# Kernel optimization log

Hardware: AMD Instinct MI355X
Metric: run time of the kernel (lower is better)

## Reference

```python
import jax, jax.numpy as jnp
import numpy as np

D_MODEL = 2048
NUM_HEADS = 16
D_KV = D_MODEL // NUM_HEADS
THETA = 10000.0


def apply_rope(x, pos):
    # x: [B, H, S, d_kv], pos: [S] int
    d = x.shape[-1]
    inv_freq = 1.0 / (THETA ** (jnp.arange(0, d, 2, dtype=jnp.float32) / d))  # [d/2]
    ang = pos.astype(jnp.float32)[:, None] * inv_freq[None, :]  # [S, d/2]
    cos, sin = jnp.cos(ang), jnp.sin(ang)  # broadcast over B,H
    x1 = x[..., 0::2]
    x2 = x[..., 1::2]
    r1 = x1 * cos - x2 * sin
    r2 = x1 * sin + x2 * cos
    return jnp.stack([r1, r2], axis=-1).reshape(x.shape)


def setup_inputs() -> dict:
    key = jax.random.key(0)
    k = jax.random.split(key, 5)
    B, S = 2, 2048
    x = jax.random.normal(k[0], (B, S, D_MODEL), dtype=jnp.float32)
    scale = 1.0 / np.sqrt(D_MODEL)
    Wq = jax.random.normal(k[1], (D_MODEL, D_MODEL), dtype=jnp.float32) * scale
    Wk = jax.random.normal(k[2], (D_MODEL, D_MODEL), dtype=jnp.float32) * scale
    Wv = jax.random.normal(k[3], (D_MODEL, D_MODEL), dtype=jnp.float32) * scale
    Wo = jax.random.normal(k[4], (D_MODEL, D_MODEL), dtype=jnp.float32) * scale
    token_position = jnp.arange(S, dtype=jnp.int64 if jax.config.jax_enable_x64 else jnp.int32)
    return {"x": x, "Wq": Wq, "Wk": Wk, "Wv": Wv, "Wo": Wo, "token_position": token_position}


def reference(x, Wq, Wk, Wv, Wo, token_position):
    B, S, _ = x.shape
    def heads(y):
        return y.reshape(B, S, NUM_HEADS, D_KV).transpose(0, 2, 1, 3)  # [B,H,S,d]
    Q = heads(jnp.einsum('bsd,df->bsf', x, Wq))
    K = heads(jnp.einsum('bsd,df->bsf', x, Wk))
    V = heads(jnp.einsum('bsd,df->bsf', x, Wv))
    Q = apply_rope(Q, token_position)
    K = apply_rope(K, token_position)
    scale = 1.0 / jnp.sqrt(jnp.asarray(D_KV, dtype=x.dtype))
    scores = jnp.einsum('bhqd,bhkd->bhqk', Q, K) * scale  # [B,H,S,S]
    causal = jnp.tril(jnp.ones((S, S), dtype=bool))
    scores = jnp.where(causal, scores, -jnp.inf)
    attn = jax.nn.softmax(scores, axis=-1)
    out = jnp.einsum('bhqk,bhkd->bhqd', attn, V)  # [B,H,S,d]
    out = out.transpose(0, 2, 1, 3).reshape(B, S, D_MODEL)
    return jnp.einsum('bsd,df->bsf', out, Wo)
```

## Files before the change

### kernel.cpp

```cpp
#include <hip/hip_runtime.h>
#include <hip/hip_bf16.h>

#define S 2048
#define DM 2048
#define NH 16
#define DH 128

typedef __attribute__((ext_vector_type(8))) short short8;
typedef __attribute__((ext_vector_type(4))) float floatx4;
typedef unsigned short u16;
typedef unsigned int u32;

__device__ __forceinline__ u16 f2bf(float f) {
  union { float f; u32 u; } v; v.f = f;
  u32 r = v.u + 0x7fffu + ((v.u >> 16) & 1u);
  return (u16)(r >> 16);
}
__device__ __forceinline__ u32 pack2(float lo, float hi) {
  float2 f; f.x = lo; f.y = hi;
  __hip_bfloat162 h = __float22bfloat162_rn(f);
  union { __hip_bfloat162 h; u32 u; } c; c.h = h;
  return c.u;
}

__device__ __forceinline__ floatx4 mfma16(short8 a, short8 b, floatx4 c) {
  return __builtin_amdgcn_mfma_f32_16x16x32_bf16(a, b, c, 0, 0, 0);
}

__device__ __forceinline__ void async_cp16(const u16* g, u16* l) {
  __builtin_amdgcn_global_load_lds(
      (const __attribute__((address_space(1))) void*)g,
      (__attribute__((address_space(3))) void*)l, 16, 0, 0);
}

__global__ void conv_x_k(const float* __restrict__ x, u16* __restrict__ xb) {
  int gid = blockIdx.x * 256 + threadIdx.x;
  float4 v = ((const float4*)x)[gid];
  uint2 p; p.x = pack2(v.x, v.y); p.y = pack2(v.z, v.w);
  ((uint2*)xb)[gid] = p;
}

__global__ void conv_w_k(const float* __restrict__ W0, const float* __restrict__ W1,
                         const float* __restrict__ W2, const float* __restrict__ W3,
                         u16* __restrict__ out) {
  __shared__ float tile[32][33];
  const float* W = blockIdx.z == 0 ? W0 : blockIdx.z == 1 ? W1 : blockIdx.z == 2 ? W2 : W3;
  u16* O = out + (size_t)blockIdx.z * DM * DM;
  int tx = threadIdx.x & 31, ty = threadIdx.x >> 5;
  int k0 = blockIdx.y * 32, n0 = blockIdx.x * 32;
#pragma unroll
  for (int j = 0; j < 4; j++)
    tile[ty + j * 8][tx] = W[(size_t)(k0 + ty + j * 8) * DM + n0 + tx];
  __syncthreads();
#pragma unroll
  for (int j = 0; j < 4; j++)
    O[(size_t)(n0 + ty + j * 8) * DM + k0 + tx] = f2bf(tile[tx][ty + j * 8]);
}

#define BM 128
#define BN 256
#define BK 64
#define NT (DM / BK)

#define BARRIER __builtin_amdgcn_s_barrier()
#define SB __builtin_amdgcn_sched_barrier(0)
#define LGKM0 asm volatile("s_waitcnt lgkmcnt(0)" ::: "memory")

#define STG_B(q, j, koff) \
  async_cp16(pBg + (size_t)(j) * 32 * DM + (koff), &Bs[q][so + (j) * 2048])
#define STG_A(q, j, koff) \
  async_cp16(pAg + (size_t)(j) * 32 * DM + (koff), &As[q][so + (j) * 2048])

#define MFMA4(mi, av) \
    acc[mi][0] = mfma16(av, b0, acc[mi][0]); \
    acc[mi][1] = mfma16(av, b1, acc[mi][1]); \
    acc[mi][2] = mfma16(av, b2, acc[mi][2]); \
    acc[mi][3] = mfma16(av, b3, acc[mi][3]);

#define PH1(p, q, koff, PRE) { \
    a0 = *(const short8*)&As[p][arow + xk0]; \
    a1 = *(const short8*)&As[p][1024 + arow + xk0]; \
    a2 = *(const short8*)&As[p][2048 + arow + xk0]; \
    a3 = *(const short8*)&As[p][3072 + arow + xk0]; \
    b0 = *(const short8*)&Bs[p][brow + xk0]; \
    b1 = *(const short8*)&Bs[p][1024 + brow + xk0]; \
    b2 = *(const short8*)&Bs[p][2048 + brow + xk0]; \
    b3 = *(const short8*)&Bs[p][3072 + brow + xk0]; \
    if (PRE) { STG_B(q, 0, koff); STG_B(q, 1, koff); STG_B(q, 2, koff); } \
    BARRIER; LGKM0; SB; \
    __builtin_amdgcn_s_setprio(1); \
    MFMA4(0, a0) MFMA4(1, a1) MFMA4(2, a2) MFMA4(3, a3) \
    __builtin_amdgcn_s_setprio(0); SB; \
    if (PRE) { asm volatile("s_waitcnt vmcnt(3)" ::: "memory"); } \
    else     { asm volatile("s_waitcnt vmcnt(0)" ::: "memory"); } \
    BARRIER; }

#define PH2(p, q, koff, PRE) { \
    a0 = *(const short8*)&As[p][4096 + arow + xk0]; \
    a1 = *(const short8*)&As[p][5120 + arow + xk0]; \
    a2 = *(const short8*)&As[p][6144 + arow + xk0]; \
    a3 = *(const short8*)&As[p][7168 + arow + xk0]; \
    if (PRE) { STG_B(q, 3, koff); STG_B(q, 4, koff); STG_B(q, 5, koff); } \
    BARRIER; LGKM0; SB; \
    __builtin_amdgcn_s_setprio(1); \
    MFMA4(4, a0) MFMA4(5, a1) MFMA4(6, a2) MFMA4(7, a3) \
    __builtin_amdgcn_s_setprio(0); \
    BARRIER; }

#define PH3(p, q, koff, PRE) { \
    a0 = *(const short8*)&As[p][arow + xk1]; \
    a1 = *(const short8*)&As[p][1024 + arow + xk1]; \
    a2 = *(const short8*)&As[p][2048 + arow + xk1]; \
    a3 = *(const short8*)&As[p][3072 + arow + xk1]; \
    b0 = *(const short8*)&Bs[p][brow + xk1]; \
    b1 = *(const short8*)&Bs[p][1024 + brow + xk1]; \
    b2 = *(const short8*)&Bs[p][2048 + brow + xk1]; \
    b3 = *(const short8*)&Bs[p][3072 + brow + xk1]; \
    if (PRE) { STG_B(q, 6, koff); STG_B(q, 7, koff); STG_A(q, 0, koff); } \
    BARRIER; LGKM0; SB; \
    __builtin_amdgcn_s_setprio(1); \
    MFMA4(0, a0) MFMA4(1, a1) MFMA4(2, a2) MFMA4(3, a3) \
    __builtin_amdgcn_s_setprio(0); \
    BARRIER; }

#define PH4(p, q, koff, PRE, LAST) { \
    a0 = *(const short8*)&As[p][4096 + arow + xk1]; \
    a1 = *(const short8*)&As[p][5120 + arow + xk1]; \
    a2 = *(const short8*)&As[p][6144 + arow + xk1]; \
    a3 = *(const short8*)&As[p][7168 + arow + xk1]; \
    if (PRE) { STG_A(q, 1, koff); STG_A(q, 2, koff); STG_A(q, 3, koff); } \
    BARRIER; LGKM0; SB; \
    __builtin_amdgcn_s_setprio(1); \
    MFMA4(4, a0) MFMA4(5, a1) MFMA4(6, a2) MFMA4(7, a3) \
    __builtin_amdgcn_s_setprio(0); SB; \
    if (!LAST) { asm volatile("s_waitcnt vmcnt(2)" ::: "memory"); BARRIER; SB; } }

#define TILE(p, q, koff, PRE, LAST) \
    PH1(p, q, koff, PRE) PH2(p, q, koff, PRE) PH3(p, q, koff, PRE) \
    PH4(p, q, koff, PRE, LAST)

__global__ __launch_bounds__(256, 1)
void gemm_k(const u16* __restrict__ A, const u16* __restrict__ Wt,
            u16* __restrict__ oQ, u16* __restrict__ oK, u16* __restrict__ oV,
            float* __restrict__ oO, const int* __restrict__ tp, int opmode)
{
  __shared__ u16 As[2][BM * BK];
  __shared__ u16 Bs[2][BN * BK];
  const int t = threadIdx.x;
  const int w = t >> 6, lane = t & 63;
  const int l16 = lane & 15, quad = lane >> 4;
  const int bid = blockIdx.y * 8 + blockIdx.x;
  const int m0 = (bid & 31) * BM, n0 = (bid >> 5) * BN;
  const u16* Bt = Wt + (size_t)(opmode == 1 ? 3 : blockIdx.z) * DM * DM;

  const int srow = t >> 3;
  const int sc = ((t & 7) ^ (srow & 7)) * 8;
  const u16* pAg = A + (size_t)(m0 + srow) * DM + sc;
  const u16* pBg = Bt + (size_t)(n0 + srow) * DM + sc;
  const int so = t * 8;

  const int arow = l16 * 64;
  const int brow = w * 4096 + l16 * 64;
  const int xk0 = ((quad) ^ (l16 & 7)) << 3;
  const int xk1 = ((4 + quad) ^ (l16 & 7)) << 3;

  floatx4 acc[8][4] = {};
  short8 a0, a1, a2, a3, b0, b1, b2, b3;

#pragma unroll
  for (int j = 0; j < 8; j++) STG_B(0, j, 0);
#pragma unroll
  for (int j = 0; j < 4; j++) STG_A(0, j, 0);
  SB;
  asm volatile("s_waitcnt vmcnt(2)" ::: "memory");
  BARRIER; SB;

  for (int it = 0; it < 15; ++it) {
    const int kA = it * 128 + 64;
    const int kB = it * 128 + 128;
    TILE(0, 1, kA, 1, 0)
    TILE(1, 0, kB, 1, 0)
  }
  TILE(0, 1, 31 * 64, 1, 0)
  TILE(1, 0, 0, 0, 1)

  const int mode = (opmode == 1) ? 3 : ((int)blockIdx.z == 2 ? 2 : 0);
  const int nbase = n0 + w * 64;
  if (mode == 3) {
#pragma unroll
    for (int mi = 0; mi < 8; mi++) {
      int m = m0 + mi * 16 + quad * 4;
#pragma unroll
      for (int ni = 0; ni < 4; ni++) {
        int n = nbase + ni * 16 + l16;
#pragma unroll
        for (int r = 0; r < 4; r++)
          oO[(size_t)(m + r) * DM + n] = acc[mi][ni][r];
      }
    }
  } else if (mode == 2) {
#pragma unroll
    for (int mi = 0; mi < 8; mi++) {
      int m = m0 + mi * 16 + quad * 4;
      int b = m >> 11, s = m & (S - 1);
#pragma unroll
      for (int ni = 0; ni < 4; ni++) {
        int f = nbase + ni * 16 + l16;
        int h = f >> 7, dh = f & (DH - 1);
        uint2 pk; pk.x = pack2(acc[mi][ni][0], acc[mi][ni][1]);
        pk.y = pack2(acc[mi][ni][2], acc[mi][ni][3]);
        *(uint2*)&oV[((size_t)(b * NH + h) * DH + dh) * S + s] = pk;
      }
    }
  } else {
    u16* Out = ((int)blockIdx.z == 0) ? oQ : oK;
    const float qs = ((int)blockIdx.z == 0) ? 0.12752780f : 1.0f;
#pragma unroll
    for (int mi = 0; mi < 8; mi++) {
#pragma unroll
      for (int r = 0; r < 4; r++) {
        int m = m0 + mi * 16 + quad * 4 + r;
        int b = m >> 11, s = m & (S - 1);
        int ps = tp[s];
#pragma unroll
        for (int ni = 0; ni < 4; ni++) {
          int f = nbase + ni * 16 + l16;
          int h = f >> 7, dh = f & (DH - 1);
          float own = acc[mi][ni][r];
          float oth = __shfl_xor(own, 1, 64);
          float fr = __expf((float)(dh & ~1) * (-9.210340371976184f / 128.0f));
          float ang = (float)ps * fr;
          float sn, cs; __sincosf(ang, &sn, &cs);
          float res = (dh & 1) ? (oth * sn + own * cs) : (own * cs - oth * sn);
          Out[((size_t)(b * NH + h) * S + s) * DH + dh] = f2bf(res * qs);
        }
      }
    }
  }
}

__global__ __launch_bounds__(256, 4)
void attn_k(const u16* __restrict__ Q, const u16* __restrict__ K,
            const u16* __restrict__ Vt, u16* __restrict__ O)
{
  __shared__ u16 Ks[64 * 128];
  __shared__ u16 Vs[128 * 64];
  __shared__ u16 P[4][16 * 64];
  const int t = threadIdx.x, w = t >> 6, lane = t & 63;
  const int l16 = lane & 15, quad = lane >> 4;
  const int task = blockIdx.x;
  const int bh = task & 31, b = bh >> 4, h = bh & 15;
  const int g = 31 - (task >> 5);
  const int qg = g * 64;
  const int qt = qg + w * 16;
  const u16* Qb = Q + (size_t)bh * S * DH;
  const u16* Kb = K + (size_t)bh * S * DH;
  const u16* Vb = Vt + (size_t)bh * DH * S;
  u16* Pw = P[w];
  const int pxor = l16 & 7;

  const u16* pK[4]; u16* lK[4];
  const u16* pV[4]; u16* lV[4];
#pragma unroll
  for (int j = 0; j < 4; j++) {
    int kr = w * 16 + j * 4 + (lane >> 4);
    int ks = lane & 15;
    int kc = ks ^ (kr & 15);
    pK[j] = Kb + (size_t)kr * DH + kc * 8;
    lK[j] = &Ks[kr * 128 + ks * 8];
    int vr = w * 32 + j * 8 + (lane >> 3);
    int vs = lane & 7;
    int vc = vs ^ (vr & 7);
    pV[j] = Vb + (size_t)vr * S + vc * 8;
    lV[j] = &Vs[vr * 64 + vs * 8];
  }

  short8 aq[4];
#pragma unroll
  for (int kc = 0; kc < 4; kc++)
    aq[kc] = *(const short8*)&Qb[(size_t)(qt + l16) * DH + kc * 32 + quad * 8];

  floatx4 o[8] = {};
  float lsum = 0.0f;
  const int kend = qg + 64;

  for (int k0 = 0; k0 < kend; k0 += 64) {
#pragma unroll
    for (int j = 0; j < 4; j++) async_cp16(pK[j] + (size_t)k0 * DH, lK[j]);
#pragma unroll
    for (int j = 0; j < 4; j++) async_cp16(pV[j] + k0, lV[j]);
    __syncthreads();

    floatx4 sc[4] = {};
#pragma unroll
    for (int hh = 0; hh < 4; hh++) {
      int row = hh * 16 + l16;
#pragma unroll
      for (int kc = 0; kc < 4; kc++) {
        short8 kf = *(short8*)&Ks[row * 128 + (((kc * 4 + quad) ^ l16) << 3)];
        sc[hh] = mfma16(kf, aq[kc], sc[hh]);
      }
    }
    if (k0 + 64 > qt) {
#pragma unroll
      for (int hh = 0; hh < 4; hh++)
#pragma unroll
        for (int r = 0; r < 4; r++) {
          int j = k0 + hh * 16 + quad * 4 + r;
          if (j > qt + l16) sc[hh][r] = -3.0e38f;
        }
    }
#pragma unroll
    for (int hh = 0; hh < 4; hh++) {
      float e0 = __builtin_amdgcn_exp2f(fminf(sc[hh][0], 44.0f));
      float e1 = __builtin_amdgcn_exp2f(fminf(sc[hh][1], 44.0f));
      float e2 = __builtin_amdgcn_exp2f(fminf(sc[hh][2], 44.0f));
      float e3 = __builtin_amdgcn_exp2f(fminf(sc[hh][3], 44.0f));
      lsum += (e0 + e1) + (e2 + e3);
      uint2 pk; pk.x = pack2(e0, e1); pk.y = pack2(e2, e3);
      int su = (2 * hh + (quad >> 1)) ^ pxor;
      *(uint2*)&Pw[l16 * 64 + su * 8 + (quad & 1) * 4] = pk;
    }
    asm volatile("s_waitcnt lgkmcnt(0)" ::: "memory");
#pragma unroll
    for (int c = 0; c < 2; c++) {
      short8 pf = *(short8*)&Pw[l16 * 64 + (((4 * c + quad) ^ pxor) << 3)];
#pragma unroll
      for (int t8 = 0; t8 < 8; t8++) {
        int row = t8 * 16 + l16;
        short8 av = *(short8*)&Vs[row * 64 + (((c * 4 + quad) ^ (l16 & 7)) << 3)];
        o[t8] = mfma16(av, pf, o[t8]);
      }
    }
    __syncthreads();
  }

  float l = lsum + __shfl_xor(lsum, 16, 64);
  l += __shfl_xor(l, 32, 64);
  float inv = __builtin_amdgcn_rcpf(l);
#pragma unroll
  for (int t8 = 0; t8 < 8; t8++) {
    uint2 pa;
    pa.x = pack2(o[t8][0] * inv, o[t8][1] * inv);
    pa.y = pack2(o[t8][2] * inv, o[t8][3] * inv);
    *(uint2*)&O[((size_t)(b * S + qt + l16)) * DM + h * DH + t8 * 16 + quad * 4] = pa;
  }
}

extern "C" void kernel_launch(void* const* d_in, const int* in_sizes, int n_in,
                              void* d_out, int out_size, void* d_ws, size_t ws_size,
                              hipStream_t stream) {
  const float* x  = (const float*)d_in[0];
  const float* Wq = (const float*)d_in[1];
  const float* Wk = (const float*)d_in[2];
  const float* Wv = (const float*)d_in[3];
  const float* Wo = (const float*)d_in[4];
  const int*   tp = (const int*)d_in[5];

  char* ws = (char*)d_ws;
  u16* Wt = (u16*)ws;
  u16* xb = (u16*)(ws + 33554432);
  u16* Qb = (u16*)(ws + 50331648);
  u16* Kb = (u16*)(ws + 67108864);
  u16* Vb = (u16*)(ws + 83886080);
  u16* Ob = (u16*)(ws + 100663296);

  conv_x_k<<<8192, 256, 0, stream>>>(x, xb);
  conv_w_k<<<dim3(64, 64, 4), 256, 0, stream>>>(Wq, Wk, Wv, Wo, Wt);
  gemm_k<<<dim3(8, 32, 3), 256, 0, stream>>>(xb, Wt, Qb, Kb, Vb, nullptr, tp, 0);
  attn_k<<<1024, 256, 0, stream>>>(Qb, Kb, Vb, Ob);
  gemm_k<<<dim3(8, 32, 1), 256, 0, stream>>>(Ob, Wt, nullptr, nullptr,
                                             nullptr, (float*)d_out, tp, 1);
}
```

Before: 418.1 us.

## Enlarge GEMM tiles to 256x256 with 8 waves in a 2x4 wave grid

The projection GEMM moves from a 128x256 block tile with 4 waves to a 256x256 tile with 8 waves (512 threads) arranged 2x4. Each wave still owns a 128x64 sub-tile, now loading both k-halves of its A and B fragments at once and interleaving the MFMAs over four phases. The aim is more operand reuse per block and fewer blocks, halving the grid. In exchange it doubles LDS per block (128 KB with the double buffer), holds more fragment registers per thread, and loses the previous bid-swizzled block ordering. It also drops the partial vmcnt waits in favour of full waits, which may expose load latency.

```diff
diff --git a/kernel.cpp b/kernel.cpp
--- a/kernel.cpp
+++ b/kernel.cpp
@@ -57,89 +57,138 @@
     O[(size_t)(n0 + ty + j * 8) * DM + k0 + tx] = f2bf(tile[tx][ty + j * 8]);
 }
 
-#define BM 128
+#define BM 256
 #define BN 256
 #define BK 64
-#define NT (DM / BK)
 
 #define BARRIER __builtin_amdgcn_s_barrier()
 #define SB __builtin_amdgcn_sched_barrier(0)
 #define LGKM0 asm volatile("s_waitcnt lgkmcnt(0)" ::: "memory")
 
+#define STG_A(q, j, koff) \
+  async_cp16(pAg + (size_t)(j) * 64 * DM + (koff), &As[q][soff + (j) * 4096])
 #define STG_B(q, j, koff) \
-  async_cp16(pBg + (size_t)(j) * 32 * DM + (koff), &Bs[q][so + (j) * 2048])
-#define STG_A(q, j, koff) \
-  async_cp16(pAg + (size_t)(j) * 32 * DM + (koff), &As[q][so + (j) * 2048])
-
-#define MFMA4(mi, av) \
-    acc[mi][0] = mfma16(av, b0, acc[mi][0]); \
-    acc[mi][1] = mfma16(av, b1, acc[mi][1]); \
-    acc[mi][2] = mfma16(av, b2, acc[mi][2]); \
-    acc[mi][3] = mfma16(av, b3, acc[mi][3]);
-
-#define PH1(p, q, koff, PRE) { \
-    a0 = *(const short8*)&As[p][arow + xk0]; \
-    a1 = *(const short8*)&As[p][1024 + arow + xk0]; \
-    a2 = *(const short8*)&As[p][2048 + arow + xk0]; \
-    a3 = *(const short8*)&As[p][3072 + arow + xk0]; \
-    b0 = *(const short8*)&Bs[p][brow + xk0]; \
-    b1 = *(const short8*)&Bs[p][1024 + brow + xk0]; \
-    b2 = *(const short8*)&Bs[p][2048 + brow + xk0]; \
-    b3 = *(const short8*)&Bs[p][3072 + brow + xk0]; \
-    if (PRE) { STG_B(q, 0, koff); STG_B(q, 1, koff); STG_B(q, 2, koff); } \
+  async_cp16(pBg + (size_t)(j) * 64 * DM + (koff), &Bs[q][soff + (j) * 4096])
+
+#define PH0(p, q, koff, PRE) { \
+    a0k0 = *(const short8*)&As[p][awb + xk0]; \
+    a0k1 = *(const short8*)&As[p][awb + xk1]; \
+    a1k0 = *(const short8*)&As[p][awb + 1024 + xk0]; \
+    a1k1 = *(const short8*)&As[p][awb + 1024 + xk1]; \
+    a2k0 = *(const short8*)&As[p][awb + 2048 + xk0]; \
+    a2k1 = *(const short8*)&As[p][awb + 2048 + xk1]; \
+    a3k0 = *(const short8*)&As[p][awb + 3072 + xk0]; \
+    a3k1 = *(const short8*)&As[p][awb + 3072 + xk1]; \
+    b0k0 = *(const short8*)&Bs[p][bwb + xk0]; \
+    b0k1 = *(const short8*)&Bs[p][bwb + xk1]; \
+    b1k0 = *(const short8*)&Bs[p][bwb + 1024 + xk0]; \
+    b1k1 = *(const short8*)&Bs[p][bwb + 1024 + xk1]; \
+    if (PRE) { STG_A(q, 0, koff); STG_A(q, 1, koff); \
+               STG_A(q, 2, koff); STG_A(q, 3, koff); } \
     BARRIER; LGKM0; SB; \
     __builtin_amdgcn_s_setprio(1); \
-    MFMA4(0, a0) MFMA4(1, a1) MFMA4(2, a2) MFMA4(3, a3) \
-    __builtin_amdgcn_s_setprio(0); SB; \
-    if (PRE) { asm volatile("s_waitcnt vmcnt(3)" ::: "memory"); } \
-    else     { asm volatile("s_waitcnt vmcnt(0)" ::: "memory"); } \
+    acc[0][0] = mfma16(a0k0, b0k0, acc[0][0]); \
+    acc[1][0] = mfma16(a1k0, b0k0, acc[1][0]); \
+    acc[2][0] = mfma16(a2k0, b0k0, acc[2][0]); \
+    acc[3][0] = mfma16(a3k0, b0k0, acc[3][0]); \
+    acc[0][1] = mfma16(a0k0, b1k0, acc[0][1]); \
+    acc[1][1] = mfma16(a1k0, b1k0, acc[1][1]); \
+    acc[2][1] = mfma16(a2k0, b1k0, acc[2][1]); \
+    acc[3][1] = mfma16(a3k0, b1k0, acc[3][1]); \
+    acc[0][0] = mfma16(a0k1, b0k1, acc[0][0]); \
+    acc[1][0] = mfma16(a1k1, b0k1, acc[1][0]); \
+    acc[2][0] = mfma16(a2k1, b0k1, acc[2][0]); \
+    acc[3][0] = mfma16(a3k1, b0k1, acc[3][0]); \
+    acc[0][1] = mfma16(a0k1, b1k1, acc[0][1]); \
+    acc[1][1] = mfma16(a1k1, b1k1, acc[1][1]); \
+    acc[2][1] = mfma16(a2k1, b1k1, acc[2][1]); \
+    acc[3][1] = mfma16(a3k1, b1k1, acc[3][1]); \
+    __builtin_amdgcn_s_setprio(0); \
     BARRIER; }
 
-#define PH2(p, q, koff, PRE) { \
-    a0 = *(const short8*)&As[p][4096 + arow + xk0]; \
-    a1 = *(const short8*)&As[p][5120 + arow + xk0]; \
-    a2 = *(const short8*)&As[p][6144 + arow + xk0]; \
-    a3 = *(const short8*)&As[p][7168 + arow + xk0]; \
-    if (PRE) { STG_B(q, 3, koff); STG_B(q, 4, koff); STG_B(q, 5, koff); } \
+#define PH1(p, q, koff, PRE) { \
+    b2k0 = *(const short8*)&Bs[p][bwb + 2048 + xk0]; \
+    b2k1 = *(const short8*)&Bs[p][bwb + 2048 + xk1]; \
+    b3k0 = *(const short8*)&Bs[p][bwb + 3072 + xk0]; \
+    b3k1 = *(const short8*)&Bs[p][bwb + 3072 + xk1]; \
+    if (PRE) { STG_B(q, 0, koff); STG_B(q, 1, koff); \
+               STG_B(q, 2, koff); STG_B(q, 3, koff); } \
     BARRIER; LGKM0; SB; \
     __builtin_amdgcn_s_setprio(1); \
-    MFMA4(4, a0) MFMA4(5, a1) MFMA4(6, a2) MFMA4(7, a3) \
+    acc[0][2] = mfma16(a0k0, b2k0, acc[0][2]); \
+    acc[1][2] = mfma16(a1k0, b2k0, acc[1][2]); \
+    acc[2][2] = mfma16(a2k0, b2k0, acc[2][2]); \
+    acc[3][2] = mfma16(a3k0, b2k0, acc[3][2]); \
+    acc[0][3] = mfma16(a0k0, b3k0, acc[0][3]); \
+    acc[1][3] = mfma16(a1k0, b3k0, acc[1][3]); \
+    acc[2][3] = mfma16(a2k0, b3k0, acc[2][3]); \
+    acc[3][3] = mfma16(a3k0, b3k0, acc[3][3]); \
+    acc[0][2] = mfma16(a0k1, b2k1, acc[0][2]); \
+    acc[1][2] = mfma16(a1k1, b2k1, acc[1][2]); \
+    acc[2][2] = mfma16(a2k1, b2k1, acc[2][2]); \
+    acc[3][2] = mfma16(a3k1, b2k1, acc[3][2]); \
+    acc[0][3] = mfma16(a0k1, b3k1, acc[0][3]); \
+    acc[1][3] = mfma16(a1k1, b3k1, acc[1][3]); \
+    acc[2][3] = mfma16(a2k1, b3k1, acc[2][3]); \
+    acc[3][3] = mfma16(a3k1, b3k1, acc[3][3]); \
     __builtin_amdgcn_s_setprio(0); \
     BARRIER; }
 
-#define PH3(p, q, koff, PRE) { \
-    a0 = *(const short8*)&As[p][arow + xk1]; \
-    a1 = *(const short8*)&As[p][1024 + arow + xk1]; \
-    a2 = *(const short8*)&As[p][2048 + arow + xk1]; \
-    a3 = *(const short8*)&As[p][3072 + arow + xk1]; \
-    b0 = *(const short8*)&Bs[p][brow + xk1]; \
-    b1 = *(const short8*)&Bs[p][1024 + brow + xk1]; \
-    b2 = *(const short8*)&Bs[p][2048 + brow + xk1]; \
-    b3 = *(const short8*)&Bs[p][3072 + brow + xk1]; \
-    if (PRE) { STG_B(q, 6, koff); STG_B(q, 7, koff); STG_A(q, 0, koff); } \
+#define PH2(p) { \
+    a0k0 = *(const short8*)&As[p][awb + 4096 + xk0]; \
+    a0k1 = *(const short8*)&As[p][awb + 4096 + xk1]; \
+    a1k0 = *(const short8*)&As[p][awb + 5120 + xk0]; \
+    a1k1 = *(const short8*)&As[p][awb + 5120 + xk1]; \
+    a2k0 = *(const short8*)&As[p][awb + 6144 + xk0]; \
+    a2k1 = *(const short8*)&As[p][awb + 6144 + xk1]; \
+    a3k0 = *(const short8*)&As[p][awb + 7168 + xk0]; \
+    a3k1 = *(const short8*)&As[p][awb + 7168 + xk1]; \
     BARRIER; LGKM0; SB; \
     __builtin_amdgcn_s_setprio(1); \
-    MFMA4(0, a0) MFMA4(1, a1) MFMA4(2, a2) MFMA4(3, a3) \
+    acc[4][0] = mfma16(a0k0, b0k0, acc[4][0]); \
+    acc[5][0] = mfma16(a1k0, b0k0, acc[5][0]); \
+    acc[6][0] = mfma16(a2k0, b0k0, acc[6][0]); \
+    acc[7][0] = mfma16(a3k0, b0k0, acc[7][0]); \
+    acc[4][1] = mfma16(a0k0, b1k0, acc[4][1]); \
+    acc[5][1] = mfma16(a1k0, b1k0, acc[5][1]); \
+    acc[6][1] = mfma16(a2k0, b1k0, acc[6][1]); \
+    acc[7][1] = mfma16(a3k0, b1k0, acc[7][1]); \
+    acc[4][0] = mfma16(a0k1, b0k1, acc[4][0]); \
+    acc[5][0] = mfma16(a1k1, b0k1, acc[5][0]); \
+    acc[6][0] = mfma16(a2k1, b0k1, acc[6][0]); \
+    acc[7][0] = mfma16(a3k1, b0k1, acc[7][0]); \
+    acc[4][1] = mfma16(a0k1, b1k1, acc[4][1]); \
+    acc[5][1] = mfma16(a1k1, b1k1, acc[5][1]); \
+    acc[6][1] = mfma16(a2k1, b1k1, acc[6][1]); \
+    acc[7][1] = mfma16(a3k1, b1k1, acc[7][1]); \
     __builtin_amdgcn_s_setprio(0); \
     BARRIER; }
 
-#define PH4(p, q, koff, PRE, LAST) { \
-    a0 = *(const short8*)&As[p][4096 + arow + xk1]; \
-    a1 = *(const short8*)&As[p][5120 + arow + xk1]; \
-    a2 = *(const short8*)&As[p][6144 + arow + xk1]; \
-    a3 = *(const short8*)&As[p][7168 + arow + xk1]; \
-    if (PRE) { STG_A(q, 1, koff); STG_A(q, 2, koff); STG_A(q, 3, koff); } \
-    BARRIER; LGKM0; SB; \
+#define PH3(PRE) { \
     __builtin_amdgcn_s_setprio(1); \
-    MFMA4(4, a0) MFMA4(5, a1) MFMA4(6, a2) MFMA4(7, a3) \
+    acc[4][2] = mfma16(a0k0, b2k0, acc[4][2]); \
+    acc[5][2] = mfma16(a1k0, b2k0, acc[5][2]); \
+    acc[6][2] = mfma16(a2k0, b2k0, acc[6][2]); \
+    acc[7][2] = mfma16(a3k0, b2k0, acc[7][2]); \
+    acc[4][3] = mfma16(a0k0, b3k0, acc[4][3]); \
+    acc[5][3] = mfma16(a1k0, b3k0, acc[5][3]); \
+    acc[6][3] = mfma16(a2k0, b3k0, acc[6][3]); \
+    acc[7][3] = mfma16(a3k0, b3k0, acc[7][3]); \
+    acc[4][2] = mfma16(a0k1, b2k1, acc[4][2]); \
+    acc[5][2] = mfma16(a1k1, b2k1, acc[5][2]); \
+    acc[6][2] = mfma16(a2k1, b2k1, acc[6][2]); \
+    acc[7][2] = mfma16(a3k1, b2k1, acc[7][2]); \
+    acc[4][3] = mfma16(a0k1, b3k1, acc[4][3]); \
+    acc[5][3] = mfma16(a1k1, b3k1, acc[5][3]); \
+    acc[6][3] = mfma16(a2k1, b3k1, acc[6][3]); \
+    acc[7][3] = mfma16(a3k1, b3k1, acc[7][3]); \
     __builtin_amdgcn_s_setprio(0); SB; \
-    if (!LAST) { asm volatile("s_waitcnt vmcnt(2)" ::: "memory"); BARRIER; SB; } }
-
-#define TILE(p, q, koff, PRE, LAST) \
-    PH1(p, q, koff, PRE) PH2(p, q, koff, PRE) PH3(p, q, koff, PRE) \
-    PH4(p, q, koff, PRE, LAST)
-
-__global__ __launch_bounds__(256, 1)
+    if (PRE) { asm volatile("s_waitcnt vmcnt(0)" ::: "memory"); BARRIER; SB; } }
+
+#define TILE(p, q, koff, PRE) \
+    PH0(p, q, koff, PRE) PH1(p, q, koff, PRE) PH2(p) PH3(PRE)
+
+__global__ __launch_bounds__(512, 2)
 void gemm_k(const u16* __restrict__ A, const u16* __restrict__ Wt,
             u16* __restrict__ oQ, u16* __restrict__ oK, u16* __restrict__ oV,
             float* __restrict__ oO, const int* __restrict__ tp, int opmode)
@@ -149,50 +198,50 @@
   const int t = threadIdx.x;
   const int w = t >> 6, lane = t & 63;
   const int l16 = lane & 15, quad = lane >> 4;
-  const int bid = blockIdx.y * 8 + blockIdx.x;
-  const int m0 = (bid & 31) * BM, n0 = (bid >> 5) * BN;
+  const int wr = w >> 2, wc = w & 3;
+  const int m0 = blockIdx.y * BM, n0 = blockIdx.x * BN;
   const u16* Bt = Wt + (size_t)(opmode == 1 ? 3 : blockIdx.z) * DM * DM;
 
   const int srow = t >> 3;
   const int sc = ((t & 7) ^ (srow & 7)) * 8;
   const u16* pAg = A + (size_t)(m0 + srow) * DM + sc;
   const u16* pBg = Bt + (size_t)(n0 + srow) * DM + sc;
-  const int so = t * 8;
-
-  const int arow = l16 * 64;
-  const int brow = w * 4096 + l16 * 64;
+  const int soff = t * 8;
+
+  const int awb = (wr * 128 + l16) * 64;
+  const int bwb = (wc * 64 + l16) * 64;
   const int xk0 = ((quad) ^ (l16 & 7)) << 3;
   const int xk1 = ((4 + quad) ^ (l16 & 7)) << 3;
 
   floatx4 acc[8][4] = {};
-  short8 a0, a1, a2, a3, b0, b1, b2, b3;
-
-#pragma unroll
-  for (int j = 0; j < 8; j++) STG_B(0, j, 0);
+  short8 a0k0, a0k1, a1k0, a1k1, a2k0, a2k1, a3k0, a3k1;
+  short8 b0k0, b0k1, b1k0, b1k1, b2k0, b2k1, b3k0, b3k1;
+
 #pragma unroll
   for (int j = 0; j < 4; j++) STG_A(0, j, 0);
+#pragma unroll
+  for (int j = 0; j < 4; j++) STG_B(0, j, 0);
   SB;
-  asm volatile("s_waitcnt vmcnt(2)" ::: "memory");
+  asm volatile("s_waitcnt vmcnt(0)" ::: "memory");
   BARRIER; SB;
 
-  for (int it = 0; it < 15; ++it) {
-    const int kA = it * 128 + 64;
-    const int kB = it * 128 + 128;
-    TILE(0, 1, kA, 1, 0)
-    TILE(1, 0, kB, 1, 0)
+  for (int it = 0; it < 16; ++it) {
+    const int kA = (2 * it + 1) * 64;
+    const int kB = (2 * it + 2) * 64;
+    TILE(0, 1, kA, 1)
+    TILE(1, 0, kB, it < 15)
   }
-  TILE(0, 1, 31 * 64, 1, 0)
-  TILE(1, 0, 0, 0, 1)
 
   const int mode = (opmode == 1) ? 3 : ((int)blockIdx.z == 2 ? 2 : 0);
-  const int nbase = n0 + w * 64;
+  const int mwb = m0 + wr * 128;
+  const int nwb = n0 + wc * 64;
   if (mode == 3) {
 #pragma unroll
     for (int mi = 0; mi < 8; mi++) {
-      int m = m0 + mi * 16 + quad * 4;
+      int m = mwb + mi * 16 + quad * 4;
 #pragma unroll
       for (int ni = 0; ni < 4; ni++) {
-        int n = nbase + ni * 16 + l16;
+        int n = nwb + ni * 16 + l16;
 #pragma unroll
         for (int r = 0; r < 4; r++)
           oO[(size_t)(m + r) * DM + n] = acc[mi][ni][r];
@@ -201,11 +250,11 @@
   } else if (mode == 2) {
 #pragma unroll
     for (int mi = 0; mi < 8; mi++) {
-      int m = m0 + mi * 16 + quad * 4;
+      int m = mwb + mi * 16 + quad * 4;
       int b = m >> 11, s = m & (S - 1);
 #pragma unroll
       for (int ni = 0; ni < 4; ni++) {
-        int f = nbase + ni * 16 + l16;
+        int f = nwb + ni * 16 + l16;
         int h = f >> 7, dh = f & (DH - 1);
         uint2 pk; pk.x = pack2(acc[mi][ni][0], acc[mi][ni][1]);
         pk.y = pack2(acc[mi][ni][2], acc[mi][ni][3]);
@@ -219,12 +268,12 @@
     for (int mi = 0; mi < 8; mi++) {
 #pragma unroll
       for (int r = 0; r < 4; r++) {
-        int m = m0 + mi * 16 + quad * 4 + r;
+        int m = mwb + mi * 16 + quad * 4 + r;
         int b = m >> 11, s = m & (S - 1);
         int ps = tp[s];
 #pragma unroll
         for (int ni = 0; ni < 4; ni++) {
-          int f = nbase + ni * 16 + l16;
+          int f = nwb + ni * 16 + l16;
           int h = f >> 7, dh = f & (DH - 1);
           float own = acc[mi][ni][r];
           float oth = __shfl_xor(own, 1, 64);
@@ -367,8 +416,8 @@
 
   conv_x_k<<<8192, 256, 0, stream>>>(x, xb);
   conv_w_k<<<dim3(64, 64, 4), 256, 0, stream>>>(Wq, Wk, Wv, Wo, Wt);
-  gemm_k<<<dim3(8, 32, 3), 256, 0, stream>>>(xb, Wt, Qb, Kb, Vb, nullptr, tp, 0);
+  gemm_k<<<dim3(8, 16, 3), 512, 0, stream>>>(xb, Wt, Qb, Kb, Vb, nullptr, tp, 0);
   attn_k<<<1024, 256, 0, stream>>>(Qb, Kb, Vb, Ob);
-  gemm_k<<<dim3(8, 32, 1), 256, 0, stream>>>(Ob, Wt, nullptr, nullptr,
+  gemm_k<<<dim3(8, 16, 1), 512, 0, stream>>>(Ob, Wt, nullptr, nullptr,
                                              nullptr, (float*)d_out, tp, 1);
 }
```

Result: faster. 388.2 us (-7.1%).
